# Performance work log

Measured on AMD Instinct MI355X. Metric: run time of the kernel, lower is better.

The kernel has to match this reference:

```python
import jax, jax.numpy as jnp
import numpy as np

B, S, HN, TN = 8, 32, 64, 512
HID, EMB, VOCAB = 512, 512, 10000


def setup_inputs():
    key = jax.random.key(0)
    k = jax.random.split(key, 14)
    w = lambda kk, shape: jax.random.normal(kk, shape, jnp.float32) * 0.02
    return {
        "dec_out": jax.random.normal(k[0], (B, S, HID), jnp.float32),
        "history": jax.random.normal(k[1], (B, HID), jnp.float32),
        "head": jax.random.randint(k[2], (B, HN), 0, VOCAB),
        "tail": jax.random.randint(k[3], (B, TN), 0, VOCAB),
        "adj_mask": jax.random.randint(k[4], (B, HN, TN), 0, 2).astype(bool),
        "dup_mask": jax.random.randint(k[5], (B, S, TN), 0, 2).astype(bool),
        "emb_table": w(k[6], (VOCAB, EMB)),
        "W_tq": w(k[7], (2 * HID + EMB, HID)),
        "b_tq": jnp.zeros((HID,), jnp.float32),
        "W_tk": w(k[8], (EMB, HID)),
        "b_tk": jnp.zeros((HID,), jnp.float32),
        "W_tout": w(k[9], (2 * HID, HID)),
        "W_hq": w(k[10], (2 * HID, HID)),
        "b_hq": jnp.zeros((HID,), jnp.float32),
        "W_hk": w(k[11], (HID, HID)),
        "b_hk": jnp.zeros((HID,), jnp.float32),
    }


def reference(dec_out, history, head, tail, adj_mask, dup_mask, emb_table,
              W_tq, b_tq, W_tk, b_tk, W_tout, W_hq, b_hq, W_hk, b_hk):
    head_emb = emb_table[head]  # (B, HN, EMB)
    tail_emb = emb_table[tail]  # (B, TN, EMB)

    # --- tail attention query: Linear(cat([dec_out, history, head_emb])) + ELU.
    # Same math as the torch broadcast-concat, computed as a sum of three
    # partial matmuls to avoid materializing the (B,S,HN,2*hid+emb) concat.
    Wd, Wh, We = W_tq[:HID], W_tq[HID:2 * HID], W_tq[2 * HID:]
    tq = jax.nn.elu((dec_out @ Wd)[:, :, None, :]
                    + (history @ Wh)[:, None, None, :]
                    + (head_emb @ We)[:, None, :, :]
                    + b_tq)                       # (B, S, HN, HID)
    tq = tq.reshape(B, S * HN, HID)
    tk = jax.nn.elu(tail_emb @ W_tk + b_tk)       # (B, TN, HID)  (dropout=eval)

    # combined logical mask: allowed = adjacency AND not-duplicate
    mask = (adj_mask[:, None, :, :] & ~dup_mask[:, :, None, :]).reshape(B, S * HN, TN)

    # GlobalAttention (dot): score -> mask -> softmax -> context -> tanh(linear_out([c;q]))
    scores = jnp.einsum('bqh,bth->bqt', tq, tk)   # (B, S*HN, TN)
    tail_attn = jax.nn.softmax(jnp.where(mask, scores, -jnp.inf), axis=-1)
    ctx = jnp.einsum('bqt,bth->bqh', tail_attn, tk)
    graph_hid = jnp.tanh(ctx @ W_tout[:HID] + tq @ W_tout[HID:])
    graph_hid = graph_hid.reshape(B * S, HN, HID)
    tail_attn = tail_attn.reshape(B * S, HN, TN)

    # --- head attention (one-step), length-masked over HN
    hq = jax.nn.elu(dec_out @ W_hq[:HID] + (history @ W_hq[HID:])[:, None, :] + b_hq)
    hq = hq.reshape(B * S, HID)
    hk = jax.nn.elu(jnp.einsum('nkh,hd->nkd', graph_hid, W_hk) + b_hk)
    lengths = jnp.repeat(jnp.sum(head != 0, axis=-1), S)          # (B*S,)
    hscores = jnp.einsum('nh,nkh->nk', hq, hk)                    # (B*S, HN)
    lmask = jnp.arange(HN)[None, :] < lengths[:, None]
    head_attn = jax.nn.softmax(jnp.where(lmask, hscores, -jnp.inf), axis=-1)
    # (head-attention context output is discarded by the original module)

    prob = jnp.einsum('nk,nkt->nt', head_attn, tail_attn).reshape(B, S, TN)
    return jnp.log(prob + 1e-20)
```

## Files before the change

### kernel.cpp

```cpp
#include <hip/hip_runtime.h>
#include <math.h>

#define BB 8
#define SS 32
#define HN 64
#define TN 512
#define HID 512

typedef __attribute__((ext_vector_type(8))) short short8;
typedef __attribute__((ext_vector_type(4))) float f32x4;

__device__ __forceinline__ float eluf(float x) { return x > 0.f ? x : (expf(x) - 1.f); }

__device__ __forceinline__ short f2bs(float f) {
    union { float f; unsigned int u; } v; v.f = f;
    unsigned int r = v.u + 0x7fffu + ((v.u >> 16) & 1u);
    return (short)(r >> 16);
}
__device__ __forceinline__ float b2f(short s) {
    union { unsigned int u; float f; } v;
    v.u = ((unsigned int)(unsigned short)s) << 16;
    return v.f;
}

__device__ __forceinline__ void gld16(const void* g, void* l) {
    __builtin_amdgcn_global_load_lds(
        (const __attribute__((address_space(1))) void*)g,
        (__attribute__((address_space(3))) void*)l, 16, 0, 0);
}

template <int ACT, int OUTB>
__device__ __forceinline__ void gcore(
    const short* __restrict__ A, const short* __restrict__ B,
    const float* __restrict__ bias, void* __restrict__ Cv,
    int ldc, int K, int m0, int n0, int cm0, short* Ls)
{
    short* Al = Ls;
    short* Bl = Ls + 8192;
    const int tid  = threadIdx.x;
    const int lane = tid & 63;
    const int w    = tid >> 6;
    const int wr   = w >> 1, wc = w & 1;
    const int l16  = lane & 15, quad = lane >> 4;

    const int srow = w * 16 + (lane >> 2);
    const int scol = (lane & 3) * 8;

    f32x4 acc[4][4];
#pragma unroll
    for (int i = 0; i < 4; ++i)
#pragma unroll
        for (int j = 0; j < 4; ++j) { acc[i][j][0]=0.f; acc[i][j][1]=0.f; acc[i][j][2]=0.f; acc[i][j][3]=0.f; }

    short* lA = Al + w * 512;
    short* lB = Bl + w * 512;
    const long rstep = (long)64 * K;

    const short* Ag = A + (long)(m0 + srow) * K + scol;
    const short* Bg = B + (long)(n0 + srow) * K + scol;
    for (int kt = 0; kt < K; kt += 64) {
        __syncthreads();
        gld16(Ag + kt, lA);
        gld16(Ag + kt + rstep, lA + 2048);
        gld16(Ag + kt + 32, lA + 4096);
        gld16(Ag + kt + 32 + rstep, lA + 4096 + 2048);
        gld16(Bg + kt, lB);
        gld16(Bg + kt + rstep, lB + 2048);
        gld16(Bg + kt + 32, lB + 4096);
        gld16(Bg + kt + 32 + rstep, lB + 4096 + 2048);
        __syncthreads();
#pragma unroll
        for (int h = 0; h < 2; ++h) {
            short8 af[4], bf4[4];
#pragma unroll
            for (int mi = 0; mi < 4; ++mi)
                af[mi] = *(const short8*)(Al + h * 4096 + (wr * 64 + mi * 16 + l16) * 32 + quad * 8);
#pragma unroll
            for (int ni = 0; ni < 4; ++ni)
                bf4[ni] = *(const short8*)(Bl + h * 4096 + (wc * 64 + ni * 16 + l16) * 32 + quad * 8);
#pragma unroll
            for (int mi = 0; mi < 4; ++mi)
#pragma unroll
                for (int ni = 0; ni < 4; ++ni)
                    acc[mi][ni] = __builtin_amdgcn_mfma_f32_16x16x32_bf16(af[mi], bf4[ni], acc[mi][ni], 0, 0, 0);
        }
    }

    __syncthreads();

    float bv[4];
#pragma unroll
    for (int ni = 0; ni < 4; ++ni)
        bv[ni] = bias ? bias[n0 + wc * 64 + ni * 16 + l16] : 0.f;

    if (OUTB == 1) {
        short* eb = Ls + w * 1152;
        const int er = lane >> 2;
        const int ec = (lane & 3) * 16;
#pragma unroll
        for (int mi = 0; mi < 4; ++mi) {
#pragma unroll
            for (int ni = 0; ni < 4; ++ni)
#pragma unroll
                for (int r = 0; r < 4; ++r) {
                    float x = acc[mi][ni][r] + bv[ni];
                    if (ACT == 1) x = eluf(x);
                    eb[(quad * 4 + r) * 72 + ni * 16 + l16] = f2bs(x);
                }
            __builtin_amdgcn_sched_barrier(0);
            short8 v0 = *(const short8*)&eb[er * 72 + ec];
            short8 v1 = *(const short8*)&eb[er * 72 + ec + 8];
            long cb = (long)(cm0 + wr * 64 + mi * 16 + er) * ldc + n0 + wc * 64 + ec;
            *(short8*)((short*)Cv + cb)     = v0;
            *(short8*)((short*)Cv + cb + 8) = v1;
            __builtin_amdgcn_sched_barrier(0);
        }
    } else {
#pragma unroll
        for (int mi = 0; mi < 4; ++mi)
#pragma unroll
            for (int ni = 0; ni < 4; ++ni) {
                int gc = n0 + wc * 64 + ni * 16 + l16;
#pragma unroll
                for (int r = 0; r < 4; ++r) {
                    float x = acc[mi][ni][r] + bv[ni];
                    if (ACT == 1) x = eluf(x);
                    ((float*)Cv)[(long)(cm0 + wr * 64 + mi * 16 + quad * 4 + r) * ldc + gc] = x;
                }
            }
    }
}

#define L_TQ   0
#define L_SC   32768
#define L_EBF  65536
#define L_HQ   75008
#define L_TOT  76032

__device__ __forceinline__ void tgemmd(
    const short* As , const short* __restrict__ B,
    f32x4 (&acc)[4][4])
{
    const int tid  = threadIdx.x;
    const int lane = tid & 63;
    const int w    = tid >> 6;
    const int l16  = lane & 15, quad = lane >> 4;
    const short* Bw = B + (long)(w * 64 + l16) * 512 + quad * 8;

#pragma unroll 2
    for (int kt = 0; kt < 512; kt += 32) {
        short8 af[4], bf[4];
#pragma unroll
        for (int ni = 0; ni < 4; ++ni)
            bf[ni] = *(const short8*)(Bw + (long)(ni * 16) * 512 + kt);
#pragma unroll
        for (int mi = 0; mi < 4; ++mi) {
            int row = mi * 16 + l16;
            int slot = ((kt >> 3) + quad) ^ (row & 7);
            af[mi] = *(const short8*)(As + row * 512 + slot * 8);
        }
#pragma unroll
        for (int mi = 0; mi < 4; ++mi)
#pragma unroll
            for (int ni = 0; ni < 4; ++ni)
                acc[mi][ni] = __builtin_amdgcn_mfma_f32_16x16x32_bf16(af[mi], bf[ni], acc[mi][ni], 0, 0, 0);
    }
}

template <int MODE>
__device__ __forceinline__ void epi(f32x4 (&acc)[4][4], short* Ls)
{
    const int tid  = threadIdx.x;
    const int lane = tid & 63;
    const int w    = tid >> 6;
    const int l16  = lane & 15, quad = lane >> 4;
    short* eb = Ls + L_EBF + w * 1152;
    const int er = lane >> 2;
    const int ec = (lane & 3) * 16;
#pragma unroll
    for (int mi = 0; mi < 4; ++mi) {
#pragma unroll
        for (int ni = 0; ni < 4; ++ni)
#pragma unroll
            for (int r = 0; r < 4; ++r) {
                float x = acc[mi][ni][r];
                if (MODE == 1) x = tanhf(x);
                eb[(quad * 4 + r) * 72 + ni * 16 + l16] = f2bs(x);
            }
        __builtin_amdgcn_sched_barrier(0);
        short8 v0 = *(const short8*)&eb[er * 72 + ec];
        short8 v1 = *(const short8*)&eb[er * 72 + ec + 8];
        int row = mi * 16 + er;
        if (MODE == 0) {
            *(short8*)(Ls + L_SC + row * 512 + w * 64 + ec)     = v0;
            *(short8*)(Ls + L_SC + row * 512 + w * 64 + ec + 8) = v1;
        } else {
            int g0 = (w * 64 + ec) >> 3;
            *(short8*)(Ls + L_TQ + row * 512 + ((g0)     ^ (row & 7)) * 8) = v0;
            *(short8*)(Ls + L_TQ + row * 512 + ((g0 + 1) ^ (row & 7)) * 8) = v1;
        }
        __builtin_amdgcn_sched_barrier(0);
    }
}

__device__ __forceinline__ void zacc(f32x4 (&acc)[4][4]) {
#pragma unroll
    for (int i = 0; i < 4; ++i)
#pragma unroll
        for (int j = 0; j < 4; ++j) { acc[i][j][0]=0.f; acc[i][j][1]=0.f; acc[i][j][2]=0.f; acc[i][j][3]=0.f; }
}

__global__ __launch_bounds__(512, 1) void tail_kernel(
    const float* __restrict__ qall, const float* __restrict__ qe,
    const float* __restrict__ b_tq, const float* __restrict__ b_hq,
    const short* __restrict__ tkb, const short* __restrict__ tkWTb,
    const short* __restrict__ WT,
    const int* __restrict__ adj, const int* __restrict__ dup,
    const int* __restrict__ head, const float* __restrict__ b_hk,
    float* __restrict__ out)
{
    __shared__ short Ls[L_TOT];
    const int tid  = threadIdx.x;
    const int lane = tid & 63;
    const int w    = tid >> 6;
    const int l16  = lane & 15, quad = lane >> 4;

    const int n = (blockIdx.x & 7) * 32 + (blockIdx.x >> 3);
    const int b = n >> 5;
    const int s = n & 31;

    const short* tkb_b  = tkb + (long)b * 262144;
    const short* tkWT_b = tkWTb + (long)b * 262144;
    const short* WT7    = WT + (size_t)7 * 262144;
    const short* WT8    = WT + (size_t)8 * 262144;
    float* HQ = (float*)(Ls + L_HQ);
    short* SC = Ls + L_SC;

    {
        const int cg = tid & 63;
        const int wg = tid >> 6;
        float4 qd0 = *(const float4*)(qall + (long)n * 2048 + cg * 8);
        float4 qd1 = *(const float4*)(qall + (long)n * 2048 + cg * 8 + 4);
        float4 qh0 = *(const float4*)(qall + (long)(256 + b) * 2048 + 1024 + cg * 8);
        float4 qh1 = *(const float4*)(qall + (long)(256 + b) * 2048 + 1024 + cg * 8 + 4);
        float4 bt0 = *(const float4*)(b_tq + cg * 8);
        float4 bt1 = *(const float4*)(b_tq + cg * 8 + 4);
        float base[8] = {qd0.x + qh0.x + bt0.x, qd0.y + qh0.y + bt0.y,
                         qd0.z + qh0.z + bt0.z, qd0.w + qh0.w + bt0.w,
                         qd1.x + qh1.x + bt1.x, qd1.y + qh1.y + bt1.y,
                         qd1.z + qh1.z + bt1.z, qd1.w + qh1.w + bt1.w};
#pragma unroll
        for (int i = 0; i < 8; ++i) {
            int h = wg * 8 + i;
            const float* er = qe + (long)(b * 64 + h) * 512 + cg * 8;
            float4 e0 = *(const float4*)er;
            float4 e1 = *(const float4*)(er + 4);
            float ev[8] = {e0.x, e0.y, e0.z, e0.w, e1.x, e1.y, e1.z, e1.w};
            short8 o;
#pragma unroll
            for (int u = 0; u < 8; ++u) o[u] = f2bs(eluf(base[u] + ev[u]));
            int slot = cg ^ (h & 7);
            *(short8*)(Ls + L_TQ + h * 512 + slot * 8) = o;
        }
        HQ[tid] = eluf(qall[(long)n * 2048 + 512 + tid]
                     + qall[(long)(256 + b) * 2048 + 1536 + tid] + b_hq[tid]);
    }
    __syncthreads();

    f32x4 acc[4][4];
    zacc(acc);

    tgemmd(Ls + L_TQ, tkb_b, acc);
    epi<0>(acc, Ls);
    __syncthreads();

    {
        const int* dupr = dup + ((long)(b * 32 + s)) * 512 + lane * 8;
        int4 d0 = *(const int4*)dupr, d1 = *(const int4*)(dupr + 4);
        int dm[8] = {d0.x, d0.y, d0.z, d0.w, d1.x, d1.y, d1.z, d1.w};
        for (int j = 0; j < 8; ++j) {
            int row = w * 8 + j;
            short8 v8 = *(const short8*)(SC + row * 512 + lane * 8);
            const int* adjr = adj + ((long)(b * 64 + row)) * 512 + lane * 8;
            int4 a0 = *(const int4*)adjr, a1 = *(const int4*)(adjr + 4);
            int am[8] = {a0.x, a0.y, a0.z, a0.w, a1.x, a1.y, a1.z, a1.w};
            float v[8];
            float m = -INFINITY;
#pragma unroll
            for (int i = 0; i < 8; ++i) {
                v[i] = (am[i] && !dm[i]) ? b2f(v8[i]) : -INFINITY;
                m = fmaxf(m, v[i]);
            }
#pragma unroll
            for (int d = 32; d >= 1; d >>= 1) m = fmaxf(m, __shfl_xor(m, d));
            float sum = 0.f;
#pragma unroll
            for (int i = 0; i < 8; ++i) {
                float e = (m == -INFINITY) ? 0.f : expf(v[i] - m);
                v[i] = e; sum += e;
            }
#pragma unroll
            for (int d = 32; d >= 1; d >>= 1) sum += __shfl_xor(sum, d);
            float inv = sum > 0.f ? 1.f / sum : 0.f;
            short8 o;
#pragma unroll
            for (int i = 0; i < 8; ++i) o[i] = f2bs(v[i] * inv);
            *(short8*)(SC + row * 512 + (lane ^ (row & 7)) * 8) = o;
        }
    }
    __syncthreads();

    zacc(acc);
    tgemmd(Ls + L_TQ, WT7, acc);
    tgemmd(SC, tkWT_b, acc);
    __syncthreads();
    epi<1>(acc, Ls);
    __syncthreads();

    zacc(acc);
    tgemmd(Ls + L_TQ, WT8, acc);

    float* F     = (float*)(Ls + L_EBF);
    float* redf  = F;
    float* hal   = F + 512;
    float* partf = F + 576;
    {
        float bv[4], hqv[4];
#pragma unroll
        for (int ni = 0; ni < 4; ++ni) {
            int col = w * 64 + ni * 16 + l16;
            bv[ni]  = b_hk[col];
            hqv[ni] = HQ[col];
        }
#pragma unroll
        for (int mi = 0; mi < 4; ++mi)
#pragma unroll
            for (int r = 0; r < 4; ++r) {
                float p = 0.f;
#pragma unroll
                for (int ni = 0; ni < 4; ++ni)
                    p += eluf(acc[mi][ni][r] + bv[ni]) * hqv[ni];
                p += __shfl_xor(p, 1);
                p += __shfl_xor(p, 2);
                p += __shfl_xor(p, 4);
                p += __shfl_xor(p, 8);
                if (l16 == 0) redf[w * 64 + mi * 16 + quad * 4 + r] = p;
            }
    }
    __syncthreads();

    if (tid < 64) {
        float sv_raw = 0.f;
#pragma unroll
        for (int w2 = 0; w2 < 8; ++w2) sv_raw += redf[w2 * 64 + tid];
        int hv = head[b * 64 + tid];
        unsigned long long ball = __ballot(hv != 0);
        int len = __popcll(ball);
        float sv = (tid < len) ? sv_raw : -INFINITY;
        float m = sv;
#pragma unroll
        for (int d = 32; d >= 1; d >>= 1) m = fmaxf(m, __shfl_xor(m, d));
        float e = expf(sv - m);
        float sum = e;
#pragma unroll
        for (int d = 32; d >= 1; d >>= 1) sum += __shfl_xor(sum, d);
        hal[tid] = e / sum;
    }
    __syncthreads();

    {
        float a2[8] = {};
#pragma unroll
        for (int k = 0; k < 8; ++k) {
            int row = w * 8 + k;
            float a = hal[row];
            short8 tv = *(const short8*)(SC + row * 512 + (lane ^ (row & 7)) * 8);
#pragma unroll
            for (int u = 0; u < 8; ++u) a2[u] += a * b2f(tv[u]);
        }
        float4* pp = (float4*)&partf[w * 512 + lane * 8];
        pp[0] = make_float4(a2[0], a2[1], a2[2], a2[3]);
        pp[1] = make_float4(a2[4], a2[5], a2[6], a2[7]);
    }
    __syncthreads();

    {
        float a = 0.f;
#pragma unroll
        for (int w2 = 0; w2 < 8; ++w2) a += partf[w2 * 512 + tid];
        out[(long)n * 512 + tid] = logf(a + 1e-20f);
    }
}

struct WTDesc { const float* src[9]; short* dst[9]; };

__global__ __launch_bounds__(256) void prep(
    const float* __restrict__ dec_out, const float* __restrict__ history,
    short* __restrict__ decb,
    const float* __restrict__ emb, const int* __restrict__ head, const int* __restrict__ tail,
    short* __restrict__ embAll, WTDesc wd)
{
    __shared__ float t[32][33];
    const int id = blockIdx.x, tid = threadIdx.x;
    if (id < 132) {
        int i = (id * 256 + tid) * 4;
        float4 v = (i < 131072) ? *(const float4*)(dec_out + i)
                                : *(const float4*)(history + (i - 131072));
        short4 o;
        o.x = f2bs(v.x); o.y = f2bs(v.y); o.z = f2bs(v.z); o.w = f2bs(v.w);
        *(short4*)(decb + i) = o;
    } else if (id < 132 + 2304) {
        int r = (id - 132) * 2 + (tid >> 7);
        int c4 = (tid & 127) * 4;
        int idx = (r < 512) ? head[r] : tail[r - 512];
        float4 v = *(const float4*)(emb + (long)idx * 512 + c4);
        short4 o;
        o.x = f2bs(v.x); o.y = f2bs(v.y); o.z = f2bs(v.z); o.w = f2bs(v.w);
        *(short4*)(embAll + (long)r * 512 + c4) = o;
    } else {
        int q = id - 2436;
        int z = q >> 8, xy = q & 255;
        int x = xy & 15, y = xy >> 4;
        const float* src = wd.src[z];
        short* dst = wd.dst[z];
        int k0 = y * 32, n0 = x * 32;
        int tx = tid & 31, ty = tid >> 5;
#pragma unroll
        for (int i = 0; i < 32; i += 8)
            t[ty + i][tx] = src[(long)(k0 + ty + i) * 512 + n0 + tx];
        __syncthreads();
#pragma unroll
        for (int i = 0; i < 32; i += 8)
            dst[(long)(n0 + ty + i) * 512 + k0 + tx] = f2bs(t[tx][ty + i]);
    }
}

__global__ __launch_bounds__(256) void mgemm_multi(
    const short* __restrict__ decb, const short* __restrict__ WTall, float* __restrict__ qall,
    const short* __restrict__ embAll, const short* __restrict__ WTe, float* __restrict__ qe,
    const short* __restrict__ WTk, const float* __restrict__ b_tk, short* __restrict__ tkb)
{
    __shared__ short Ls[16384];
    int id = blockIdx.x;
    if (id < 48) {
        int y = id >> 4, x = id & 15;
        gcore<0, 0>(decb, WTall, nullptr, qall, 2048, 512, y * 128, x * 128, y * 128, Ls);
    } else if (id < 64) {
        int id2 = id - 48, y = id2 >> 2, x = id2 & 3;
        gcore<0, 0>(embAll, WTe, nullptr, qe, 512, 512, y * 128, x * 128, y * 128, Ls);
    } else {
        int id3 = id - 64, y = id3 >> 2, x = id3 & 3;
        gcore<1, 1>(embAll, WTk, b_tk, tkb, 512, 512, 512 + y * 128, x * 128, y * 128, Ls);
    }
}

__global__ __launch_bounds__(256) void tkwt_kernel(
    const short* __restrict__ WTo1, const short* __restrict__ tkb, short* __restrict__ tkWTb)
{
    __shared__ short Ls[16384];
    int id = blockIdx.x;
    int z = id >> 4, r = id & 15;
    int x = r & 3, y = r >> 2;
    gcore<0, 1>(WTo1, tkb + (long)z * 262144, nullptr,
                tkWTb + (long)z * 262144, 512, 512, y * 128, x * 128, y * 128, Ls);
}

extern "C" void kernel_launch(void* const* d_in, const int* in_sizes, int n_in,
                              void* d_out, int out_size, void* d_ws, size_t ws_size,
                              hipStream_t stream)
{
    const float* dec_out = (const float*)d_in[0];
    const float* history = (const float*)d_in[1];
    const int*   head    = (const int*)d_in[2];
    const int*   tail    = (const int*)d_in[3];
    const int*   adj     = (const int*)d_in[4];
    const int*   dup     = (const int*)d_in[5];
    const float* emb     = (const float*)d_in[6];
    const float* W_tq    = (const float*)d_in[7];
    const float* b_tq    = (const float*)d_in[8];
    const float* W_tk    = (const float*)d_in[9];
    const float* b_tk    = (const float*)d_in[10];
    const float* W_tout  = (const float*)d_in[11];
    const float* W_hq    = (const float*)d_in[12];
    const float* b_hq    = (const float*)d_in[13];
    const float* W_hk    = (const float*)d_in[14];
    const float* b_hk    = (const float*)d_in[15];
    float* out = (float*)d_out;

    char* ws = (char*)d_ws;
    auto alloc = [&](size_t bytes) -> void* {
        char* p = ws;
        ws += (bytes + 255) & ~(size_t)255;
        return (void*)p;
    };
    short* decb   = (short*)alloc((size_t)384 * 512 * 2);
    short* embAll = (short*)alloc((size_t)4608 * 512 * 2);
    short* WT     = (short*)alloc((size_t)9 * 512 * 512 * 2);
    float* qall   = (float*)alloc((size_t)384 * 2048 * 4);
    float* qe     = (float*)alloc((size_t)512 * 512 * 4);
    short* tkb    = (short*)alloc((size_t)4096 * 512 * 2);
    short* tkWTb  = (short*)alloc((size_t)4096 * 512 * 2);

    WTDesc wd;
    wd.src[0] = W_tq;               wd.dst[0] = WT;
    wd.src[1] = W_hq;               wd.dst[1] = WT + (size_t)1 * 262144;
    wd.src[2] = W_tq + 512 * 512;   wd.dst[2] = WT + (size_t)2 * 262144;
    wd.src[3] = W_hq + 512 * 512;   wd.dst[3] = WT + (size_t)3 * 262144;
    wd.src[4] = W_tq + 1024 * 512;  wd.dst[4] = WT + (size_t)4 * 262144;
    wd.src[5] = W_tk;               wd.dst[5] = WT + (size_t)5 * 262144;
    wd.src[6] = W_tout;             wd.dst[6] = WT + (size_t)6 * 262144;
    wd.src[7] = W_tout + 512 * 512; wd.dst[7] = WT + (size_t)7 * 262144;
    wd.src[8] = W_hk;               wd.dst[8] = WT + (size_t)8 * 262144;

    prep<<<4740, 256, 0, stream>>>(dec_out, history, decb, emb, head, tail, embAll, wd);
    mgemm_multi<<<192, 256, 0, stream>>>(decb, WT, qall, embAll, WT + (size_t)4 * 262144, qe,
                                         WT + (size_t)5 * 262144, b_tk, tkb);
    tkwt_kernel<<<128, 256, 0, stream>>>(WT + (size_t)6 * 262144, tkb, tkWTb);
    tail_kernel<<<256, 512, 0, stream>>>(qall, qe, b_tq, b_hq, tkb, tkWTb, WT,
                                         adj, dup, head, b_hk, out);
}
```

Measured before the change: 215.9 us.

## Stage B tiles through double-buffered LDS and reorder GEMMs to reuse tq

Adds a GEMM variant that streams the global B operand into a double-buffered LDS staging area with async loads and barriers, replacing direct per-wave global reads for three of the four GEMMs. The tq@W_tout[HID:] GEMM is moved ahead of the scores GEMM into a second accumulator, which frees the tq LDS region early so it can double as the staging buffer for the context GEMM. The aim is to overlap global loads with MFMA work and share B tiles across waves, at the cost of more register pressure (two accumulator sets) and extra block barriers per k-step.

```diff
diff --git a/kernel.cpp b/kernel.cpp
--- a/kernel.cpp
+++ b/kernel.cpp
@@ -131,15 +131,70 @@
     }
 }
 
-#define L_TQ   0
-#define L_SC   32768
-#define L_EBF  65536
+#define L_R1   0
+#define L_R2   32768
+#define L_EB   65536
 #define L_HQ   75008
 #define L_TOT  76032
 
+__device__ __forceinline__ void tgemms(
+    const short* As, const short* __restrict__ B, short* ST, f32x4 (&acc)[4][4])
+{
+    const int tid  = threadIdx.x;
+    const int lane = tid & 63;
+    const int w    = tid >> 6;
+    const int l16  = lane & 15, quad = lane >> 4;
+
+    auto STAGE = [&](int kt, int p) {
+        short* Bl = ST + p * 16384;
+#pragma unroll
+        for (int j = 0; j < 4; ++j) {
+            int lin = j * 512 + tid;
+            int r = lin >> 2, gs = lin & 3;
+            int g = gs ^ ((r >> 1) & 3);
+            gld16(B + (long)r * 512 + kt + g * 8, Bl + j * 4096 + w * 512);
+        }
+    };
+
+    STAGE(0, 0);
+    int p = 0;
+    for (int kt = 0; kt < 512; kt += 32, p ^= 1) {
+        if (kt + 32 < 512) {
+            STAGE(kt + 32, p ^ 1);
+            asm volatile("s_waitcnt vmcnt(4)" ::: "memory");
+        } else {
+            asm volatile("s_waitcnt vmcnt(0)" ::: "memory");
+        }
+        __builtin_amdgcn_s_barrier();
+        __builtin_amdgcn_sched_barrier(0);
+
+        short* Bl = ST + p * 16384;
+        short8 af[4], bf[4];
+#pragma unroll
+        for (int mi = 0; mi < 4; ++mi) {
+            int row = mi * 16 + l16;
+            int slot = ((kt >> 3) + quad) ^ (row & 7);
+            af[mi] = *(const short8*)(As + row * 512 + slot * 8);
+        }
+#pragma unroll
+        for (int ni = 0; ni < 4; ++ni) {
+            int row = w * 64 + ni * 16 + l16;
+            int slot = quad ^ ((row >> 1) & 3);
+            bf[ni] = *(const short8*)(Bl + row * 32 + slot * 8);
+        }
+#pragma unroll
+        for (int mi = 0; mi < 4; ++mi)
+#pragma unroll
+            for (int ni = 0; ni < 4; ++ni)
+                acc[mi][ni] = __builtin_amdgcn_mfma_f32_16x16x32_bf16(af[mi], bf[ni], acc[mi][ni], 0, 0, 0);
+        asm volatile("s_waitcnt lgkmcnt(0)" ::: "memory");
+        __builtin_amdgcn_s_barrier();
+        __builtin_amdgcn_sched_barrier(0);
+    }
+}
+
 __device__ __forceinline__ void tgemmd(
-    const short* As , const short* __restrict__ B,
-    f32x4 (&acc)[4][4])
+    const short* As, const short* __restrict__ B, f32x4 (&acc)[4][4])
 {
     const int tid  = threadIdx.x;
     const int lane = tid & 63;
@@ -174,7 +229,7 @@
     const int lane = tid & 63;
     const int w    = tid >> 6;
     const int l16  = lane & 15, quad = lane >> 4;
-    short* eb = Ls + L_EBF + w * 1152;
+    short* eb = Ls + L_EB + w * 1152;
     const int er = lane >> 2;
     const int ec = (lane & 3) * 16;
 #pragma unroll
@@ -192,12 +247,12 @@
         short8 v1 = *(const short8*)&eb[er * 72 + ec + 8];
         int row = mi * 16 + er;
         if (MODE == 0) {
-            *(short8*)(Ls + L_SC + row * 512 + w * 64 + ec)     = v0;
-            *(short8*)(Ls + L_SC + row * 512 + w * 64 + ec + 8) = v1;
+            *(short8*)(Ls + L_R2 + row * 512 + w * 64 + ec)     = v0;
+            *(short8*)(Ls + L_R2 + row * 512 + w * 64 + ec + 8) = v1;
         } else {
             int g0 = (w * 64 + ec) >> 3;
-            *(short8*)(Ls + L_TQ + row * 512 + ((g0)     ^ (row & 7)) * 8) = v0;
-            *(short8*)(Ls + L_TQ + row * 512 + ((g0 + 1) ^ (row & 7)) * 8) = v1;
+            *(short8*)(Ls + L_R1 + row * 512 + ((g0)     ^ (row & 7)) * 8) = v0;
+            *(short8*)(Ls + L_R1 + row * 512 + ((g0 + 1) ^ (row & 7)) * 8) = v1;
         }
         __builtin_amdgcn_sched_barrier(0);
     }
@@ -234,7 +289,7 @@
     const short* WT7    = WT + (size_t)7 * 262144;
     const short* WT8    = WT + (size_t)8 * 262144;
     float* HQ = (float*)(Ls + L_HQ);
-    short* SC = Ls + L_SC;
+    short* SC = Ls + L_R2;
 
     {
         const int cg = tid & 63;
@@ -260,18 +315,19 @@
 #pragma unroll
             for (int u = 0; u < 8; ++u) o[u] = f2bs(eluf(base[u] + ev[u]));
             int slot = cg ^ (h & 7);
-            *(short8*)(Ls + L_TQ + h * 512 + slot * 8) = o;
+            *(short8*)(Ls + L_R1 + h * 512 + slot * 8) = o;
         }
         HQ[tid] = eluf(qall[(long)n * 2048 + 512 + tid]
                      + qall[(long)(256 + b) * 2048 + 1536 + tid] + b_hq[tid]);
     }
     __syncthreads();
 
-    f32x4 acc[4][4];
-    zacc(acc);
-
-    tgemmd(Ls + L_TQ, tkb_b, acc);
-    epi<0>(acc, Ls);
+    f32x4 acc1[4][4], acc2[4][4];
+    zacc(acc1); zacc(acc2);
+
+    tgemms(Ls + L_R1, WT7,   Ls + L_R2, acc2);
+    tgemms(Ls + L_R1, tkb_b, Ls + L_R2, acc1);
+    epi<0>(acc1, Ls);
     __syncthreads();
 
     {
@@ -310,17 +366,15 @@
     }
     __syncthreads();
 
-    zacc(acc);
-    tgemmd(Ls + L_TQ, WT7, acc);
-    tgemmd(SC, tkWT_b, acc);
-    __syncthreads();
-    epi<1>(acc, Ls);
-    __syncthreads();
-
-    zacc(acc);
-    tgemmd(Ls + L_TQ, WT8, acc);
-
-    float* F     = (float*)(Ls + L_EBF);
+    tgemms(SC, tkWT_b, Ls + L_R1, acc2);
+    epi<1>(acc2, Ls);
+    __syncthreads();
+
+    zacc(acc1);
+    tgemmd(Ls + L_R1, WT8, acc1);
+    __syncthreads();
+
+    float* F     = (float*)(Ls + L_R1);
     float* redf  = F;
     float* hal   = F + 512;
     float* partf = F + 576;
@@ -339,7 +393,7 @@
                 float p = 0.f;
 #pragma unroll
                 for (int ni = 0; ni < 4; ++ni)
-                    p += eluf(acc[mi][ni][r] + bv[ni]) * hqv[ni];
+                    p += eluf(acc1[mi][ni][r] + bv[ni]) * hqv[ni];
                 p += __shfl_xor(p, 1);
                 p += __shfl_xor(p, 2);
                 p += __shfl_xor(p, 4);
```

Result: slower. 252.3 us (+16.9%).
